# Kernel optimization log

Measured on AMD Instinct MI355X. Metric: run time of the kernel, lower is better.

## Reference

```python
import jax, jax.numpy as jnp
import numpy as np

N = 65536      # nodes
E = 1048576    # edges (avg in-degree ~16)
C = 128        # in_channels = out_channels = edge_dim
T = 4          # towers
F_IN = C // T  # 32 (divide_input=True)
F_OUT = C // T # 32

# degree histogram from the repo: degrees 1..6 with these counts
_counts = np.array([108477, 299931, 180702, 10767, 3, 2], dtype=np.float64)
_degs = np.arange(1, 7, dtype=np.float64)
AVG_LIN = float((_counts * _degs).sum() / _counts.sum())
AVG_LOG = float((_counts * np.log(_degs + 1.0)).sum() / _counts.sum())


def setup_inputs() -> dict:
    key = jax.random.key(0)
    ks = jax.random.split(key, 8)
    def w(k, shape, fan_in):
        return (jax.random.normal(k, shape, jnp.float32) / np.sqrt(fan_in)).astype(jnp.float32)
    return {
        "x": jax.random.normal(ks[0], (N, C), jnp.float32),
        "edge_attr": jax.random.normal(ks[1], (E, C), jnp.float32),
        "edge_index": jax.random.randint(ks[2], (2, E), 0, N, jnp.int32),
        "W_edge": w(ks[3], (F_IN, C), C),
        "b_edge": jnp.zeros((F_IN,), jnp.float32),
        "W_pre": w(ks[4], (T, 3 * F_IN, F_IN), 3 * F_IN),
        "b_pre": jnp.zeros((T, F_IN), jnp.float32),
        "W_post": w(ks[5], (T, 13 * F_IN, F_OUT), 13 * F_IN),
        "b_post": jnp.zeros((T, F_OUT), jnp.float32),
        "W_lin": w(ks[6], (C, C), C),
        "b_lin": jnp.zeros((C,), jnp.float32),
    }


def reference(x, edge_attr, edge_index, W_edge, b_edge, W_pre, b_pre, W_post, b_post, W_lin, b_lin):
    src, dst = edge_index[0], edge_index[1]  # PyG: messages from src (x_j) aggregated at dst (x_i)
    xt = x.reshape(N, T, F_IN)               # divide_input=True: split channels across towers

    # edge encoder, broadcast across towers
    e = edge_attr @ W_edge.T + b_edge        # [E, F_in]
    e = jnp.broadcast_to(e[:, None, :], (E, T, F_IN))

    # message: gather + concat + per-tower pretrans Linear
    h = jnp.concatenate([xt[dst], xt[src], e], axis=-1)      # [E, T, 3F]
    m = jnp.einsum('etf,tfg->etg', h, W_pre) + b_pre          # [E, T, F]

    # multi-aggregator scatter-reduce over destination nodes
    cnt = jax.ops.segment_sum(jnp.ones((E,), m.dtype), dst, N)    # in-degree [N]
    cnt_safe = jnp.maximum(cnt, 1.0)[:, None, None]
    msum = jax.ops.segment_sum(m, dst, N)
    mean = msum / cnt_safe
    mean_sq = jax.ops.segment_sum(m * m, dst, N) / cnt_safe
    std = jnp.sqrt(jax.nn.relu(mean_sq - mean * mean) + 1e-5)
    empty = (cnt == 0)[:, None, None]
    mx = jnp.where(empty, 0.0, jax.ops.segment_max(m, dst, N))
    mn = jnp.where(empty, 0.0, jax.ops.segment_min(m, dst, N))
    agg = jnp.concatenate([mean, mx, mn, std], axis=-1)       # [N, T, 4F]

    # degree scalers: identity, amplification, attenuation
    deg = cnt[:, None, None]
    logd = jnp.log(deg + 1.0)
    amp = agg * (logd / AVG_LOG)
    att = agg * jnp.where(deg == 0, 1.0, AVG_LOG / jnp.where(deg == 0, 1.0, logd))
    out = jnp.concatenate([agg, amp, att], axis=-1)           # [N, T, 12F]

    # posttrans: concat self features, per-tower Linear, merge towers
    out = jnp.concatenate([xt, out], axis=-1)                 # [N, T, 13F]
    out = jnp.einsum('ntf,tfg->ntg', out, W_post) + b_post    # [N, T, F_out]
    out = out.reshape(N, C)
    return out @ W_lin.T + b_lin + x  # residual
```

## Files before the change

kernel.cpp:

```cpp
#include <hip/hip_runtime.h>
#include <math.h>

__global__ __launch_bounds__(256) void pre_kernel(
    const float* __restrict__ x, const float* __restrict__ W_pre,
    float* __restrict__ ps)
{
  __shared__ float xl[2][128];
  const int tid = threadIdx.x;
  const int nl  = tid >> 7;
  const int j   = tid & 127;
  const int n   = blockIdx.x * 2 + nl;
  xl[nl][j] = x[(size_t)n * 128 + j];
  __syncthreads();
  const int t = j >> 5, g = j & 31;
  const float* xp = &xl[nl][t * 32];
  const float* Ws = W_pre + (size_t)(t * 96 + 32) * 32 + g;
  float aps = 0.f;
#pragma unroll
  for (int f = 0; f < 32; ++f) aps += xp[f] * Ws[f * 32];
  ps[(size_t)n * 128 + j] = aps;
}

__global__ __launch_bounds__(256) void count_kernel(
    const int* __restrict__ ei, int* __restrict__ cnt, int E)
{
  const int e = blockIdx.x * 256 + threadIdx.x;
  if (e < E) atomicAdd(&cnt[ei[E + e]], 1);
}

__global__ __launch_bounds__(256) void scan_kernel(
    const int* __restrict__ cnt, int* __restrict__ base, int* __restrict__ fill)
{
  __shared__ int part[256];
  const int tid = threadIdx.x;
  const int c0 = tid * 256;
  int s = 0;
  for (int i = 0; i < 256; ++i) s += cnt[c0 + i];
  part[tid] = s;
  __syncthreads();
  if (tid == 0) {
    int run = 0;
    for (int i = 0; i < 256; ++i) { int t = part[i]; part[i] = run; run += t; }
  }
  __syncthreads();
  int run = part[tid];
  for (int i = 0; i < 256; ++i) {
    int cc = cnt[c0 + i];
    base[c0 + i] = run;
    fill[c0 + i] = run;
    run += cc;
  }
}

__global__ __launch_bounds__(256) void escatter_kernel(
    const float* __restrict__ edge_attr, const int* __restrict__ ei,
    const float* __restrict__ W_edge, const float* __restrict__ b_edge,
    int* __restrict__ fill, int* __restrict__ srcs_s,
    float* __restrict__ e_sorted, int E)
{
  __shared__ float sEA[4][2][128];
  const int tid  = threadIdx.x;
  const int lane = tid & 63;
  const int w    = tid >> 6;
  const int g    = lane & 31;
  const int half = lane >> 5;
  const int e4   = (blockIdx.x * 4 + w) * 4;
  if (e4 >= E) return;
  const int nv = min(4, E - e4);

  float we[64];
  {
    const float4* wrow = (const float4*)(W_edge + (size_t)g * 128 + half * 64);
#pragma unroll
    for (int k = 0; k < 16; ++k) {
      const float4 q = wrow[k];
      we[4*k] = q.x; we[4*k+1] = q.y; we[4*k+2] = q.z; we[4*k+3] = q.w;
    }
  }
  const float bedge = b_edge[g];

  int slot = 0;
  if (lane < nv) {
    const int e = e4 + lane;
    const int d = ei[E + e];
    const int s = ei[e];
    slot = atomicAdd(&fill[d], 1);
    srcs_s[slot] = s;
  }

  float2 va[4];
#pragma unroll
  for (int l = 0; l < 4; ++l) {
    const int el = (l < nv) ? (e4 + l) : e4;
    va[l] = *(const float2*)(edge_attr + (size_t)el * 128 + lane * 2);
  }

#pragma unroll
  for (int l = 0; l < 4; ++l) {
    if (l >= nv) break;
    *(float2*)&sEA[w][l & 1][lane * 2] = va[l];
    float acc = 0.f;
    const float4* eap = (const float4*)&sEA[w][l & 1][half * 64];
#pragma unroll
    for (int k = 0; k < 16; ++k) {
      const float4 q = eap[k];
      acc += q.x * we[4*k] + q.y * we[4*k+1] + q.z * we[4*k+2] + q.w * we[4*k+3];
    }
    acc += __shfl_xor(acc, 32);
    const int sl = __shfl(slot, l);
    if (half == 0) e_sorted[(size_t)sl * 32 + g] = acc + bedge;
  }
}

__global__ __launch_bounds__(256) void agg_kernel(
    const float* __restrict__ x,
    const float* __restrict__ W_pre, const float* __restrict__ b_pre,
    const float* __restrict__ ps, const float* __restrict__ e_sorted,
    const int* __restrict__ srcs_s, const int* __restrict__ cnt,
    const int* __restrict__ base, float* __restrict__ aggs)
{
  __shared__ float sE[4][2][64];
  __shared__ float sX[4][128];
  const int tid  = threadIdx.x;
  const int lane = tid & 63;
  const int w    = tid >> 6;
  const int g    = lane & 31;
  const int half = lane >> 5;
  const int t0   = half;
  const int n    = blockIdx.x * 4 + w;

  float wp0[32], wp1[32];
#pragma unroll
  for (int f = 0; f < 32; ++f) {
    wp0[f] = W_pre[(size_t)(t0 * 96 + 64 + f) * 32 + g];
    wp1[f] = W_pre[(size_t)((t0 + 2) * 96 + 64 + f) * 32 + g];
  }

  sX[w][lane]      = x[(size_t)n * 128 + lane];
  sX[w][lane + 64] = x[(size_t)n * 128 + 64 + lane];
  float pd0 = b_pre[t0 * 32 + g];
  float pd1 = b_pre[(t0 + 2) * 32 + g];
#pragma unroll
  for (int f = 0; f < 32; ++f) {
    pd0 += sX[w][t0 * 32 + f]       * W_pre[(size_t)(t0 * 96 + f) * 32 + g];
    pd1 += sX[w][(t0 + 2) * 32 + f] * W_pre[(size_t)((t0 + 2) * 96 + f) * 32 + g];
  }

  const int c  = cnt[n];
  const int b0 = base[n];
  float sum0 = 0.f, sum1 = 0.f, sq0 = 0.f, sq1 = 0.f;
  float mx0 = -INFINITY, mx1 = -INFINITY, mn0 = INFINITY, mn1 = INFINITY;

  float ev = 0.f, pA0 = 0.f, pA1 = 0.f, pB0 = 0.f, pB1 = 0.f;
  if (c > 0) {
    const int cm = c - 1;
    ev = e_sorted[(size_t)(b0 + min(half, cm)) * 32 + g];
    const int sA = srcs_s[b0];
    const int sB = srcs_s[b0 + min(1, cm)];
    pA0 = ps[(size_t)sA * 128 + lane];
    pA1 = ps[(size_t)sA * 128 + 64 + lane];
    pB0 = ps[(size_t)sB * 128 + lane];
    pB1 = ps[(size_t)sB * 128 + 64 + lane];
  }

  for (int i = 0; i < c; i += 2) {
    const int buf = (i >> 1) & 1;
    const int cm  = c - 1;
    const float ev_n = e_sorted[(size_t)(b0 + min(i + 2 + half, cm)) * 32 + g];
    const int sAn = srcs_s[b0 + min(i + 2, cm)];
    const int sBn = srcs_s[b0 + min(i + 3, cm)];
    const float pA0n = ps[(size_t)sAn * 128 + lane];
    const float pA1n = ps[(size_t)sAn * 128 + 64 + lane];
    const float pB0n = ps[(size_t)sBn * 128 + lane];
    const float pB1n = ps[(size_t)sBn * 128 + 64 + lane];

    sE[w][buf][lane] = ev;

    {
      float a0 = 0.f, a1 = 0.f;
      const float4* ep = (const float4*)&sE[w][buf][0];
#pragma unroll
      for (int k = 0; k < 8; ++k) {
        const float4 q = ep[k];
        a0 += q.x * wp0[4*k] + q.y * wp0[4*k+1] + q.z * wp0[4*k+2] + q.w * wp0[4*k+3];
        a1 += q.x * wp1[4*k] + q.y * wp1[4*k+1] + q.z * wp1[4*k+2] + q.w * wp1[4*k+3];
      }
      const float m0 = a0 + pd0 + pA0;
      const float m1 = a1 + pd1 + pA1;
      sum0 += m0; sq0 += m0 * m0; mx0 = fmaxf(mx0, m0); mn0 = fminf(mn0, m0);
      sum1 += m1; sq1 += m1 * m1; mx1 = fmaxf(mx1, m1); mn1 = fminf(mn1, m1);
    }
    if (i + 1 < c) {
      float a0 = 0.f, a1 = 0.f;
      const float4* ep = (const float4*)&sE[w][buf][32];
#pragma unroll
      for (int k = 0; k < 8; ++k) {
        const float4 q = ep[k];
        a0 += q.x * wp0[4*k] + q.y * wp0[4*k+1] + q.z * wp0[4*k+2] + q.w * wp0[4*k+3];
        a1 += q.x * wp1[4*k] + q.y * wp1[4*k+1] + q.z * wp1[4*k+2] + q.w * wp1[4*k+3];
      }
      const float m0 = a0 + pd0 + pB0;
      const float m1 = a1 + pd1 + pB1;
      sum0 += m0; sq0 += m0 * m0; mx0 = fmaxf(mx0, m0); mn0 = fminf(mn0, m0);
      sum1 += m1; sq1 += m1 * m1; mx1 = fmaxf(mx1, m1); mn1 = fminf(mn1, m1);
    }
    ev = ev_n; pA0 = pA0n; pA1 = pA1n; pB0 = pB0n; pB1 = pB1n;
  }

  const float csafe = fmaxf((float)c, 1.f);
  const float mean0 = sum0 / csafe, mean1 = sum1 / csafe;
  const float sd0 = sqrtf(fmaxf(sq0 / csafe - mean0 * mean0, 0.f) + 1e-5f);
  const float sd1 = sqrtf(fmaxf(sq1 / csafe - mean1 * mean1, 0.f) + 1e-5f);
  if (c == 0) { mx0 = mx1 = mn0 = mn1 = 0.f; }
  float* ag = aggs + (size_t)n * 512;
  ag[lane]       = mean0; ag[64 + lane]  = mean1;
  ag[128 + lane] = mx0;   ag[192 + lane] = mx1;
  ag[256 + lane] = mn0;   ag[320 + lane] = mn1;
  ag[384 + lane] = sd0;   ag[448 + lane] = sd1;
}

__global__ __launch_bounds__(256) void post_kernel(
    const float* __restrict__ x, const float* __restrict__ aggs,
    const int* __restrict__ cnt,
    const float* __restrict__ W_post, const float* __restrict__ b_post,
    const float* __restrict__ W_lin, const float* __restrict__ b_lin,
    float* __restrict__ out, float avg_log)
{
  __shared__ float vec[8][4][416];
  __shared__ float h2[8][128];
  const int tid = threadIdx.x;
  const int j = tid & 127;
  const int t = j >> 5, g = j & 31;
  const int n0 = blockIdx.x * 8;

  for (int itn = 0; itn < 4; ++itn) {
    const int nl = itn * 2 + (tid >> 7);
    const int n = n0 + nl;
    const size_t o = (size_t)n * 128 + j;
    const float* ag = aggs + (size_t)n * 512;
    const float c = (float)cnt[n];
    const float mean = ag[j];
    const float mx   = ag[128 + j];
    const float mn   = ag[256 + j];
    const float sd   = ag[384 + j];
    const float logd = logf(c + 1.f);
    const float amp_s = logd / avg_log;
    const float att_s = (c == 0.f) ? 1.f : (avg_log / logd);
    float* v = vec[nl][t];
    v[g]        = x[o];
    v[32 + g]   = mean;          v[64 + g]   = mx;
    v[96 + g]   = mn;            v[128 + g]  = sd;
    v[160 + g]  = mean * amp_s;  v[192 + g]  = mx * amp_s;
    v[224 + g]  = mn * amp_s;    v[256 + g]  = sd * amp_s;
    v[288 + g]  = mean * att_s;  v[320 + g]  = mx * att_s;
    v[352 + g]  = mn * att_s;    v[384 + g]  = sd * att_s;
  }
  __syncthreads();

  {
    const int nlb = tid >> 7;
    const float b = b_post[t * 32 + g];
    float acc0 = b, acc1 = b, acc2 = b, acc3 = b;
    const float* Wp = W_post + (size_t)(t * 416) * 32 + g;
    const float* v0 = vec[nlb + 0][t];
    const float* v1 = vec[nlb + 2][t];
    const float* v2 = vec[nlb + 4][t];
    const float* v3 = vec[nlb + 6][t];
    for (int f = 0; f < 416; ++f) {
      const float wv = Wp[(size_t)f * 32];
      acc0 += v0[f] * wv; acc1 += v1[f] * wv;
      acc2 += v2[f] * wv; acc3 += v3[f] * wv;
    }
    h2[nlb + 0][j] = acc0; h2[nlb + 2][j] = acc1;
    h2[nlb + 4][j] = acc2; h2[nlb + 6][j] = acc3;
  }
  __syncthreads();

  {
    const int nlb = tid >> 7;
    const float* Wl = W_lin + (size_t)j * 128;
    const float bl = b_lin[j];
    float a0 = bl, a1 = bl, a2 = bl, a3 = bl;
    const float* h0 = h2[nlb + 0];
    const float* h1 = h2[nlb + 2];
    const float* hp = h2[nlb + 4];
    const float* h3 = h2[nlb + 6];
    for (int k = 0; k < 128; ++k) {
      const float wv = Wl[k];
      a0 += h0[k] * wv; a1 += h1[k] * wv;
      a2 += hp[k] * wv; a3 += h3[k] * wv;
    }
    const size_t b0 = (size_t)(n0 + nlb + 0) * 128 + j;
    const size_t b1 = (size_t)(n0 + nlb + 2) * 128 + j;
    const size_t b2 = (size_t)(n0 + nlb + 4) * 128 + j;
    const size_t b3 = (size_t)(n0 + nlb + 6) * 128 + j;
    out[b0] = a0 + x[b0];
    out[b1] = a1 + x[b1];
    out[b2] = a2 + x[b2];
    out[b3] = a3 + x[b3];
  }
}

extern "C" void kernel_launch(void* const* d_in, const int* in_sizes, int n_in,
                              void* d_out, int out_size, void* d_ws, size_t ws_size,
                              hipStream_t stream) {
  const float* x         = (const float*)d_in[0];
  const float* edge_attr = (const float*)d_in[1];
  const int*   ei        = (const int*)  d_in[2];
  const float* W_edge    = (const float*)d_in[3];
  const float* b_edge    = (const float*)d_in[4];
  const float* W_pre     = (const float*)d_in[5];
  const float* b_pre     = (const float*)d_in[6];
  const float* W_post    = (const float*)d_in[7];
  const float* b_post    = (const float*)d_in[8];
  const float* W_lin     = (const float*)d_in[9];
  const float* b_lin     = (const float*)d_in[10];
  float* out = (float*)d_out;

  const int N = in_sizes[0] / 128;
  const int E = in_sizes[2] / 2;

  float* ps       = (float*)d_ws;
  float* aggs     = ps + (size_t)N * 128;
  float* e_sorted = aggs + (size_t)N * 512;
  int*   srcs_s   = (int*)(e_sorted + (size_t)E * 32);
  int*   cnt      = srcs_s + E;
  int*   base     = cnt + N;
  int*   fill     = base + N;

  hipMemsetAsync(cnt, 0, (size_t)N * 4, stream);

  const double counts[6] = {108477.0, 299931.0, 180702.0, 10767.0, 3.0, 2.0};
  double num = 0.0, den = 0.0;
  for (int i = 0; i < 6; ++i) { num += counts[i] * log((double)(i + 2)); den += counts[i]; }
  const float avg_log = (float)(num / den);

  pre_kernel<<<N / 2, 256, 0, stream>>>(x, W_pre, ps);
  count_kernel<<<(E + 255) / 256, 256, 0, stream>>>(ei, cnt, E);
  scan_kernel<<<1, 256, 0, stream>>>(cnt, base, fill);
  escatter_kernel<<<(E + 15) / 16, 256, 0, stream>>>(edge_attr, ei, W_edge, b_edge,
                                                     fill, srcs_s, e_sorted, E);
  agg_kernel<<<N / 4, 256, 0, stream>>>(x, W_pre, b_pre, ps, e_sorted,
                                        srcs_s, cnt, base, aggs);
  post_kernel<<<N / 8, 256, 0, stream>>>(x, aggs, cnt, W_post, b_post,
                                         W_lin, b_lin, out, avg_log);
}
```

Baseline: 1.846 ms.

## Batch 16 edges per wave in edge encoder and vectorize post-transform weights

The edge encoder now handles 16 edges per wave instead of 4 and stages edge_attr rows into LDS with global_load_lds DMA. Each weight register is then reused across 16 rows, which is meant to cut global load overhead and per-edge instruction count. A new kernel transposes W_post so the post-transform matmul can read float4 weights contiguously, and the W_lin loop and the scan's count reduction are vectorized to float4/int4 as well. This adds one small launch and a larger LDS footprint in escatter, which may lower occupancy.

```diff
diff --git a/kernel.cpp b/kernel.cpp
--- a/kernel.cpp
+++ b/kernel.cpp
@@ -35,7 +35,8 @@
   const int tid = threadIdx.x;
   const int c0 = tid * 256;
   int s = 0;
-  for (int i = 0; i < 256; ++i) s += cnt[c0 + i];
+  const int4* c4 = (const int4*)(cnt + c0);
+  for (int i = 0; i < 64; ++i) { const int4 v = c4[i]; s += v.x + v.y + v.z + v.w; }
   part[tid] = s;
   __syncthreads();
   if (tid == 0) {
@@ -52,21 +53,32 @@
   }
 }
 
+__global__ __launch_bounds__(256) void wpt_kernel(
+    const float* __restrict__ W_post, float* __restrict__ WpT)
+{
+  const int i = blockIdx.x * 256 + threadIdx.x;
+  if (i >= 4 * 416 * 32) return;
+  const int g = i & 31;
+  const int f = (i >> 5) % 416;
+  const int t = i / (416 * 32);
+  WpT[((size_t)t * 32 + g) * 416 + f] = W_post[((size_t)t * 416 + f) * 32 + g];
+}
+
 __global__ __launch_bounds__(256) void escatter_kernel(
     const float* __restrict__ edge_attr, const int* __restrict__ ei,
     const float* __restrict__ W_edge, const float* __restrict__ b_edge,
     int* __restrict__ fill, int* __restrict__ srcs_s,
     float* __restrict__ e_sorted, int E)
 {
-  __shared__ float sEA[4][2][128];
+  __shared__ float sEA[4][16][128];
   const int tid  = threadIdx.x;
   const int lane = tid & 63;
   const int w    = tid >> 6;
   const int g    = lane & 31;
   const int half = lane >> 5;
-  const int e4   = (blockIdx.x * 4 + w) * 4;
-  if (e4 >= E) return;
-  const int nv = min(4, E - e4);
+  const int e0   = (blockIdx.x * 4 + w) * 16;
+  if (e0 >= E) return;
+  const int nv = min(16, E - e0);
 
   float we[64];
   {
@@ -81,34 +93,62 @@
 
   int slot = 0;
   if (lane < nv) {
-    const int e = e4 + lane;
+    const int e = e0 + lane;
     const int d = ei[E + e];
     const int s = ei[e];
     slot = atomicAdd(&fill[d], 1);
     srcs_s[slot] = s;
   }
 
-  float2 va[4];
-#pragma unroll
-  for (int l = 0; l < 4; ++l) {
-    const int el = (l < nv) ? (e4 + l) : e4;
-    va[l] = *(const float2*)(edge_attr + (size_t)el * 128 + lane * 2);
-  }
-
-#pragma unroll
-  for (int l = 0; l < 4; ++l) {
-    if (l >= nv) break;
-    *(float2*)&sEA[w][l & 1][lane * 2] = va[l];
-    float acc = 0.f;
-    const float4* eap = (const float4*)&sEA[w][l & 1][half * 64];
+  if (nv == 16) {
+    const char* gbase = (const char*)(edge_attr + (size_t)e0 * 128) + (size_t)lane * 16;
+    char* lbase = (char*)&sEA[w][0][0];
+#pragma unroll
+    for (int inst = 0; inst < 8; ++inst) {
+      __builtin_amdgcn_global_load_lds(
+          (const __attribute__((address_space(1))) void*)(gbase + inst * 1024),
+          (__attribute__((address_space(3))) void*)(lbase + inst * 1024),
+          16, 0, 0);
+    }
+    asm volatile("s_waitcnt vmcnt(0)" ::: "memory");
+  } else {
+    for (int r = 0; r < nv; ++r)
+      *(float2*)&sEA[w][r][lane * 2] =
+          *(const float2*)(edge_attr + (size_t)(e0 + r) * 128 + lane * 2);
+  }
+
+  float acc[16];
+#pragma unroll
+  for (int r = 0; r < 16; ++r) acc[r] = 0.f;
+
+  if (nv == 16) {
 #pragma unroll
     for (int k = 0; k < 16; ++k) {
-      const float4 q = eap[k];
-      acc += q.x * we[4*k] + q.y * we[4*k+1] + q.z * we[4*k+2] + q.w * we[4*k+3];
-    }
-    acc += __shfl_xor(acc, 32);
-    const int sl = __shfl(slot, l);
-    if (half == 0) e_sorted[(size_t)sl * 32 + g] = acc + bedge;
+      const float w0 = we[4*k], w1 = we[4*k+1], w2 = we[4*k+2], w3 = we[4*k+3];
+#pragma unroll
+      for (int r = 0; r < 16; ++r) {
+        const float4 q = *(const float4*)&sEA[w][r][half * 64 + k * 4];
+        acc[r] += q.x * w0 + q.y * w1 + q.z * w2 + q.w * w3;
+      }
+    }
+  } else {
+    for (int r = 0; r < nv; ++r) {
+      float a = 0.f;
+#pragma unroll
+      for (int k = 0; k < 16; ++k) {
+        const float4 q = *(const float4*)&sEA[w][r][half * 64 + k * 4];
+        a += q.x * we[4*k] + q.y * we[4*k+1] + q.z * we[4*k+2] + q.w * we[4*k+3];
+      }
+      acc[r] = a;
+    }
+  }
+
+#pragma unroll
+  for (int r = 0; r < 16; ++r) {
+    if (r >= nv) break;
+    const float v = acc[r] + __shfl_xor(acc[r], 32);
+    const int sl = __shfl(slot, r);
+    if (half == 0) e_sorted[(size_t)sl * 32 + g] = v + bedge;
   }
 }
 
@@ -222,7 +262,7 @@
 __global__ __launch_bounds__(256) void post_kernel(
     const float* __restrict__ x, const float* __restrict__ aggs,
     const int* __restrict__ cnt,
-    const float* __restrict__ W_post, const float* __restrict__ b_post,
+    const float* __restrict__ WpT, const float* __restrict__ b_post,
     const float* __restrict__ W_lin, const float* __restrict__ b_lin,
     float* __restrict__ out, float avg_log)
 {
@@ -261,15 +301,18 @@
     const int nlb = tid >> 7;
     const float b = b_post[t * 32 + g];
     float acc0 = b, acc1 = b, acc2 = b, acc3 = b;
-    const float* Wp = W_post + (size_t)(t * 416) * 32 + g;
-    const float* v0 = vec[nlb + 0][t];
-    const float* v1 = vec[nlb + 2][t];
-    const float* v2 = vec[nlb + 4][t];
-    const float* v3 = vec[nlb + 6][t];
-    for (int f = 0; f < 416; ++f) {
-      const float wv = Wp[(size_t)f * 32];
-      acc0 += v0[f] * wv; acc1 += v1[f] * wv;
-      acc2 += v2[f] * wv; acc3 += v3[f] * wv;
+    const float4* Wp4 = (const float4*)(WpT + ((size_t)t * 32 + g) * 416);
+    const float4* v0 = (const float4*)vec[nlb + 0][t];
+    const float4* v1 = (const float4*)vec[nlb + 2][t];
+    const float4* v2 = (const float4*)vec[nlb + 4][t];
+    const float4* v3 = (const float4*)vec[nlb + 6][t];
+    for (int f = 0; f < 104; ++f) {
+      const float4 wv = Wp4[f];
+      const float4 a = v0[f], bb = v1[f], cc = v2[f], dd = v3[f];
+      acc0 += a.x  * wv.x + a.y  * wv.y + a.z  * wv.z + a.w  * wv.w;
+      acc1 += bb.x * wv.x + bb.y * wv.y + bb.z * wv.z + bb.w * wv.w;
+      acc2 += cc.x * wv.x + cc.y * wv.y + cc.z * wv.z + cc.w * wv.w;
+      acc3 += dd.x * wv.x + dd.y * wv.y + dd.z * wv.z + dd.w * wv.w;
     }
     h2[nlb + 0][j] = acc0; h2[nlb + 2][j] = acc1;
     h2[nlb + 4][j] = acc2; h2[nlb + 6][j] = acc3;
@@ -278,17 +321,20 @@
 
   {
     const int nlb = tid >> 7;
-    const float* Wl = W_lin + (size_t)j * 128;
+    const float4* Wl4 = (const float4*)(W_lin + (size_t)j * 128);
     const float bl = b_lin[j];
     float a0 = bl, a1 = bl, a2 = bl, a3 = bl;
-    const float* h0 = h2[nlb + 0];
-    const float* h1 = h2[nlb + 2];
-    const float* hp = h2[nlb + 4];
-    const float* h3 = h2[nlb + 6];
-    for (int k = 0; k < 128; ++k) {
-      const float wv = Wl[k];
-      a0 += h0[k] * wv; a1 += h1[k] * wv;
-      a2 += hp[k] * wv; a3 += h3[k] * wv;
+    const float4* h04 = (const float4*)h2[nlb + 0];
+    const float4* h14 = (const float4*)h2[nlb + 2];
+    const float4* h24 = (const float4*)h2[nlb + 4];
+    const float4* h34 = (const float4*)h2[nlb + 6];
+    for (int k = 0; k < 32; ++k) {
+      const float4 wv = Wl4[k];
+      const float4 a = h04[k], bb = h14[k], cc = h24[k], dd = h34[k];
+      a0 += a.x  * wv.x + a.y  * wv.y + a.z  * wv.z + a.w  * wv.w;
+      a1 += bb.x * wv.x + bb.y * wv.y + bb.z * wv.z + bb.w * wv.w;
+      a2 += cc.x * wv.x + cc.y * wv.y + cc.z * wv.z + cc.w * wv.w;
+      a3 += dd.x * wv.x + dd.y * wv.y + dd.z * wv.z + dd.w * wv.w;
     }
     const size_t b0 = (size_t)(n0 + nlb + 0) * 128 + j;
     const size_t b1 = (size_t)(n0 + nlb + 2) * 128 + j;
@@ -327,6 +373,7 @@
   int*   cnt      = srcs_s + E;
   int*   base     = cnt + N;
   int*   fill     = base + N;
+  float* WpT      = (float*)(fill + N);
 
   hipMemsetAsync(cnt, 0, (size_t)N * 4, stream);
 
@@ -335,13 +382,14 @@
   for (int i = 0; i < 6; ++i) { num += counts[i] * log((double)(i + 2)); den += counts[i]; }
   const float avg_log = (float)(num / den);
 
+  wpt_kernel<<<(4 * 416 * 32 + 255) / 256, 256, 0, stream>>>(W_post, WpT);
   pre_kernel<<<N / 2, 256, 0, stream>>>(x, W_pre, ps);
   count_kernel<<<(E + 255) / 256, 256, 0, stream>>>(ei, cnt, E);
   scan_kernel<<<1, 256, 0, stream>>>(cnt, base, fill);
-  escatter_kernel<<<(E + 15) / 16, 256, 0, stream>>>(edge_attr, ei, W_edge, b_edge,
+  escatter_kernel<<<(E + 63) / 64, 256, 0, stream>>>(edge_attr, ei, W_edge, b_edge,
                                                      fill, srcs_s, e_sorted, E);
   agg_kernel<<<N / 4, 256, 0, stream>>>(x, W_pre, b_pre, ps, e_sorted,
                                         srcs_s, cnt, base, aggs);
-  post_kernel<<<N / 8, 256, 0, stream>>>(x, aggs, cnt, W_post, b_post,
+  post_kernel<<<N / 8, 256, 0, stream>>>(x, aggs, cnt, WpT, b_post,
                                          W_lin, b_lin, out, avg_log);
 }
```

Measured after the change: 1.777 ms. -3.7%, faster.
